# Optimization experiments

Measured on AMD Instinct MI355X. Metric: run time of the kernel, lower is better.

Reference implementation:

```python
import jax, jax.numpy as jnp
import numpy as np

B, L, C = 4, 4096, 512
G = 4            # n_groups
H = 16           # n_heads
K = 5            # offset conv kernel == offset_range_factor
GC = C // G      # n_group_channels = 128
HC = C // H      # n_head_channels = 32


def conv1d(x, w, b, pad):
    # x: [N, Cin, L], w: [Cout, Cin, K]
    out = jax.lax.conv_general_dilated(
        x, w, window_strides=(1,), padding=[(pad, pad)],
        dimension_numbers=('NCH', 'OIH', 'NCH'))
    return out + b[None, :, None]


def grid_sample_1d(feats, gy):
    # feats: [Bg, d, L]  gy: [Bg, N] normalized coords in [-1, 1]
    # bilinear, zeros padding, align_corners=False (matches F.grid_sample)
    Bg, d, Lf = feats.shape
    N = gy.shape[-1]
    iy = ((gy + 1.0) * Lf - 1.0) * 0.5
    i0 = jnp.floor(iy)
    w1 = iy - i0
    i0 = i0.astype(jnp.int32)

    def gather(idx):
        valid = ((idx >= 0) & (idx < Lf)).astype(feats.dtype)
        idxc = jnp.clip(idx, 0, Lf - 1)
        g = jnp.take_along_axis(
            feats, jnp.broadcast_to(idxc[:, None, :], (Bg, d, N)), axis=2)
        return g * valid[:, None, :]

    return gather(i0) * (1.0 - w1)[:, None, :] + gather(i0 + 1) * w1[:, None, :]


def setup_inputs() -> dict:
    key = jax.random.key(0)
    ks = jax.random.split(key, 16)
    s = 0.02
    return {
        'x':     jax.random.normal(ks[0], (B, L, C), jnp.float32),
        'Wq':    jax.random.normal(ks[1], (C, C), jnp.float32) * s,
        'bq':    jnp.zeros((C,), jnp.float32),
        'Wk':    jax.random.normal(ks[2], (C, C), jnp.float32) * s,
        'bk':    jnp.zeros((C,), jnp.float32),
        'Wv':    jax.random.normal(ks[3], (C, C), jnp.float32) * s,
        'bv':    jnp.zeros((C,), jnp.float32),
        'Woff1': jax.random.normal(ks[4], (GC, GC, K), jnp.float32) * s,
        'boff1': jnp.zeros((GC,), jnp.float32),
        'Woff2': jax.random.normal(ks[5], (1, GC, 1), jnp.float32) * s,
        'boff2': jnp.zeros((1,), jnp.float32),
        'rpb':   jax.random.normal(ks[6], (1, C, L), jnp.float32) * s,
        'Wout':  jax.random.normal(ks[7], (C, C), jnp.float32) * s,
        'bout':  jnp.zeros((C,), jnp.float32),
    }


def reference(x, Wq, bq, Wk, bk, Wv, bv, Woff1, boff1, Woff2, boff2, rpb, Wout, bout):
    Bx, Lx, Cx = x.shape
    xc = x.transpose(0, 2, 1)                                # [B, C, L]
    # 1x1 conv projections == channel matmuls
    q = jnp.einsum('oc,bcl->bol', Wq, xc) + bq[None, :, None]
    # group queries: 'b (g d) n -> (b g) d n'
    qg = q.reshape(Bx * G, GC, Lx)
    # offset prediction: conv(k=5,pad=2) then conv(k=1,pad=2) -> length L+4
    off = conv1d(qg, Woff1, boff1, pad=K // 2)               # [Bg, GC, L]
    off = conv1d(off, Woff2, boff2, pad=K // 2)[:, 0, :]     # [Bg, L+4]
    off = jnp.tanh(off) * float(K)                           # offset_range_factor
    N = off.shape[-1]
    vgrid = jnp.arange(N, dtype=x.dtype) + off               # [Bg, L+4]
    gy = 2.0 * vgrid / float(max(N - 1, 1)) - 1.0
    # bilinear gather of grouped x, then crop to L
    xg = xc.reshape(Bx * G, GC, Lx)
    xs = grid_sample_1d(xg, gy)[:, :, :Lx]                   # [Bg, GC, L]
    xs = xs.reshape(Bx, Cx, Lx)                              # '(b g) d n -> b (g d) n'
    k = jnp.einsum('oc,bcl->bol', Wk, xs) + bk[None, :, None]
    v = jnp.einsum('oc,bcl->bol', Wv, xs) + bv[None, :, None] + rpb
    # heads: [B*H, HC, L]; attention over the CHANNEL dim (i,j = head channels)
    qh = q.reshape(Bx * H, HC, Lx)
    kh = k.reshape(Bx * H, HC, Lx)
    vh = v.reshape(Bx * H, HC, Lx)
    logits = jnp.einsum('bil,bjl->bij', qh, kh) * (Cx ** -0.5)  # [BH, HC, HC]
    attn = jax.nn.softmax(logits, axis=-1)
    o = jnp.einsum('bij,bjl->bil', attn, vh)                 # [BH, HC, L]
    # '(b g) l c -> b c (g l)' with g=H, l=HC, c=L  ->  [B, L, C]
    o = o.reshape(Bx, H, HC, Lx).transpose(0, 3, 1, 2).reshape(Bx, Lx, Cx)
    return o @ Wout.T + bout
```

## Files before the change

### kernel.cpp

```cpp
#include <hip/hip_runtime.h>
#include <math.h>

#define BB   4
#define LL   4096
#define CC   512
#define GG   4
#define HH   16
#define KW   5
#define GCC  128
#define HCC  32
#define BGN  (BB*GG)
#define BHN  (BB*HH)
#define KSPLIT 16

typedef __attribute__((ext_vector_type(8))) __bf16 bf16x8;
typedef __attribute__((ext_vector_type(4))) float f32x4;

__device__ __forceinline__ unsigned int f2bf_bits(float f) {
    unsigned int u = __float_as_uint(f);
    return (u + 0x7FFFu + ((u >> 16) & 1u)) >> 16;
}
__device__ __forceinline__ float bfbits2f(unsigned int s) {
    return __uint_as_float(s << 16);
}
__device__ __forceinline__ void split2(float v, unsigned short& h, unsigned short& l) {
    unsigned int hb = f2bf_bits(v);
    float hf = bfbits2f(hb);
    unsigned int lb = f2bf_bits(v - hf);
    h = (unsigned short)hb; l = (unsigned short)lb;
}

__device__ __forceinline__ void gload16(const void* g, void* l) {
    __builtin_amdgcn_global_load_lds(
        (const __attribute__((address_space(1))) void*)g,
        (__attribute__((address_space(3))) void*)l, 16, 0, 0);
}

__global__ __launch_bounds__(256) void split_x_kernel(
    const float* __restrict__ in, unsigned short* __restrict__ hi,
    unsigned short* __restrict__ lo, int n4)
{
    int i = blockIdx.x * 256 + threadIdx.x;
    if (i >= n4) return;
    float4 v = ((const float4*)in)[i];
    ushort4 h, l;
    split2(v.x, h.x, l.x); split2(v.y, h.y, l.y);
    split2(v.z, h.z, l.z); split2(v.w, h.w, l.w);
    ((ushort4*)hi)[i] = h;
    ((ushort4*)lo)[i] = l;
}

__global__ __launch_bounds__(256) void split_w_kernel(
    const float* __restrict__ W0, const float* __restrict__ W1,
    const float* __restrict__ W2, const float* __restrict__ W3,
    unsigned short* __restrict__ hi, unsigned short* __restrict__ lo)
{
    int w = blockIdx.y;
    const float* W = (w == 0) ? W0 : (w == 1) ? W1 : (w == 2) ? W2 : W3;
    size_t seg4 = (size_t)w * 65536;
    int i = blockIdx.x * 256 + threadIdx.x;
    float4 v = ((const float4*)W)[i];
    ushort4 h, l;
    split2(v.x, h.x, l.x); split2(v.y, h.y, l.y);
    split2(v.z, h.z, l.z); split2(v.w, h.w, l.w);
    ((ushort4*)hi)[seg4 + i] = h;
    ((ushort4*)lo)[seg4 + i] = l;
}

__global__ __launch_bounds__(256) void gemm_split_mfma(
    const unsigned short* __restrict__ Ahi, const unsigned short* __restrict__ Alo,
    const unsigned short* __restrict__ Ahi2, const unsigned short* __restrict__ Alo2,
    const unsigned short* __restrict__ Bhi, const unsigned short* __restrict__ Blo,
    const float* __restrict__ bias, const float* __restrict__ bias2,
    const float* __restrict__ rpb,
    float* __restrict__ out, float* __restrict__ out2, int ySplit,
    int RA, int RB, int Kd, size_t aStride, size_t bStride, int biasOnCol)
{
    __shared__ unsigned short sm[4][4096];

    const int b  = blockIdx.z;
    const int c0 = blockIdx.x * 128;

    int rblk = blockIdx.y;
    const unsigned short* Ah_ = Ahi;
    const unsigned short* Al_ = Alo;
    const float* bias_ = bias;
    const float* rpb_  = nullptr;
    float* out_ = out;
    if (rblk >= ySplit) {
        rblk -= ySplit;
        Ah_ = Ahi2; Al_ = Alo2; bias_ = bias2; out_ = out2; rpb_ = rpb;
    }
    const int r0 = rblk * 128;

    const int tid  = threadIdx.x;
    const int lane = tid & 63;
    const int wv   = tid >> 6;
    const int wr   = wv >> 1, wc = wv & 1;

    const int srow   = lane >> 2;
    const int schunk = (lane & 3) ^ ((lane >> 3) & 3);
    const size_t laneA = (size_t)(r0 + wv * 32 + srow) * Kd + (size_t)(schunk * 8);
    const size_t laneB = (size_t)(c0 + wv * 32 + srow) * Kd + (size_t)(schunk * 8);
    const unsigned short* gAh = Ah_ + (size_t)b * aStride + laneA;
    const unsigned short* gAl = Al_ + (size_t)b * aStride + laneA;
    const unsigned short* gBh = Bhi + (size_t)b * bStride + laneB;
    const unsigned short* gBl = Blo + (size_t)b * bStride + laneB;
    const size_t rowskip = (size_t)16 * Kd;
    const int ldsOff = wv * 1024;

    const int lr = lane & 15;
    const int kx = ((lane >> 4) ^ ((lane >> 1) & 3)) * 8;
    const int aOff = (wr * 64 + lr) * 32 + kx;
    const int bOff = (wc * 64 + lr) * 32 + kx;

    f32x4 acc[4][4];
#pragma unroll
    for (int i = 0; i < 4; ++i)
#pragma unroll
        for (int j = 0; j < 4; ++j) acc[i][j] = (f32x4){0.f, 0.f, 0.f, 0.f};

    bf16x8 ah[4], al[4], bh[4], bl[4];

    for (int k0 = 0; k0 < Kd; k0 += 32) {
        gload16(gAh + k0, &sm[0][ldsOff]);
        gload16(gAh + k0 + rowskip, &sm[0][ldsOff + 512]);
        gload16(gAl + k0, &sm[1][ldsOff]);
        gload16(gAl + k0 + rowskip, &sm[1][ldsOff + 512]);
        gload16(gBh + k0, &sm[2][ldsOff]);
        gload16(gBh + k0 + rowskip, &sm[2][ldsOff + 512]);
        gload16(gBl + k0, &sm[3][ldsOff]);
        gload16(gBl + k0 + rowskip, &sm[3][ldsOff + 512]);
        __syncthreads();

        const unsigned short* mAh = &sm[0][aOff];
        const unsigned short* mAl = &sm[1][aOff];
        const unsigned short* mBh = &sm[2][bOff];
        const unsigned short* mBl = &sm[3][bOff];
#pragma unroll
        for (int i = 0; i < 4; ++i) {
            ah[i] = *(const bf16x8*)(mAh + i * 512);
            al[i] = *(const bf16x8*)(mAl + i * 512);
        }
#pragma unroll
        for (int j = 0; j < 4; ++j) {
            bh[j] = *(const bf16x8*)(mBh + j * 512);
            bl[j] = *(const bf16x8*)(mBl + j * 512);
        }
#pragma unroll
        for (int i = 0; i < 4; ++i)
#pragma unroll
            for (int j = 0; j < 4; ++j) {
                acc[i][j] = __builtin_amdgcn_mfma_f32_16x16x32_bf16(ah[i], bh[j], acc[i][j], 0, 0, 0);
                acc[i][j] = __builtin_amdgcn_mfma_f32_16x16x32_bf16(al[i], bh[j], acc[i][j], 0, 0, 0);
                acc[i][j] = __builtin_amdgcn_mfma_f32_16x16x32_bf16(ah[i], bl[j], acc[i][j], 0, 0, 0);
            }
        __syncthreads();
    }

    const int lg4 = (lane >> 4) * 4;
    float bcol[4];
#pragma unroll
    for (int fj = 0; fj < 4; ++fj)
        bcol[fj] = biasOnCol ? bias_[c0 + wc * 64 + fj * 16 + lr] : 0.f;

#pragma unroll
    for (int fi = 0; fi < 4; ++fi) {
#pragma unroll
        for (int reg = 0; reg < 4; ++reg) {
            const int r = r0 + wr * 64 + fi * 16 + lg4 + reg;
            const float br = biasOnCol ? 0.f : bias_[r];
            float* orow = out_ + ((size_t)b * RA + r) * RB + c0;
            const float* prow = rpb_ ? (rpb_ + (size_t)r * RB + c0) : nullptr;
#pragma unroll
            for (int fj = 0; fj < 4; ++fj) {
                const int c = wc * 64 + fj * 16 + lr;
                float val = acc[fi][fj][reg] + br + bcol[fj];
                if (prow) val += prow[c];
                orow[c] = val;
            }
        }
    }
}

__global__ void comb_weights(const float* __restrict__ Woff1, const float* __restrict__ boff1,
                             const float* __restrict__ Woff2, const float* __restrict__ boff2,
                             float* __restrict__ wc)
{
    int idx = blockIdx.x * 256 + threadIdx.x;
    if (idx < GCC * KW) {
        int cp = idx / KW, t = idx - cp * KW;
        float s = 0.f;
        for (int c = 0; c < GCC; ++c)
            s = fmaf(Woff2[c], Woff1[((size_t)c * GCC + cp) * KW + t], s);
        wc[idx] = s;
    } else if (idx == GCC * KW) {
        float s = boff2[0];
        for (int c = 0; c < GCC; ++c) s = fmaf(Woff2[c], boff1[c], s);
        wc[idx] = s;
    } else if (idx == GCC * KW + 1) {
        wc[idx] = boff2[0];
    }
}

#define OLT 128
__global__ __launch_bounds__(128) void offsets_part_kernel(
    const float* __restrict__ q, const float* __restrict__ wc,
    float* __restrict__ part)
{
    __shared__ float sq[32][140];
    __shared__ float sw[32 * KW];

    const int l0 = blockIdx.x * OLT;
    const int bg = blockIdx.y;
    const int cg = blockIdx.z;
    const int tid = threadIdx.x;

    const float* qb = q + ((size_t)bg * GCC + cg * 32) * LL;

    for (int i = tid; i < 32 * KW; i += 128) sw[i] = wc[cg * 32 * KW + i];

    {
        const int row = tid >> 2;
        const int l4  = tid & 3;
        const float* qrow = qb + (size_t)row * LL + l0 - 8;
        for (int j = l4; j < 34; j += 4) {
            int idx = j * 4;
            float4 v;
            if (l0 - 8 + idx >= 0) v = *(const float4*)(qrow + idx);
            else v = make_float4(0.f, 0.f, 0.f, 0.f);
            *(float4*)&sq[row][idx] = v;
        }
    }
    __syncthreads();

    const int li = tid;
    float acc = 0.f;
#pragma unroll
    for (int cp = 0; cp < 32; ++cp) {
        const float* r  = &sq[cp][li + 4];
        const float* wr = &sw[cp * KW];
        acc = fmaf(wr[0], r[0], acc);
        acc = fmaf(wr[1], r[1], acc);
        acc = fmaf(wr[2], r[2], acc);
        acc = fmaf(wr[3], r[3], acc);
        acc = fmaf(wr[4], r[4], acc);
    }
    part[((size_t)cg * BGN + bg) * LL + l0 + li] = acc;
}

__global__ __launch_bounds__(256) void offsets_finish_kernel(
    const float* __restrict__ part, const float* __restrict__ wc,
    float* __restrict__ offv)
{
    int i = blockIdx.x * 256 + threadIdx.x;
    int bg = i >> 12;
    int l  = i & (LL - 1);
    float acc;
    if (l < 2) {
        acc = wc[GCC * KW + 1];
    } else {
        acc = wc[GCC * KW]
            + part[((size_t)0 * BGN + bg) * LL + l]
            + part[((size_t)1 * BGN + bg) * LL + l]
            + part[((size_t)2 * BGN + bg) * LL + l]
            + part[((size_t)3 * BGN + bg) * LL + l];
    }
    float off = tanhf(acc) * (float)KW;
    float vg  = (float)l + off;
    float iy  = vg * ((float)LL / (float)(LL + 2 * (KW / 2) - 1)) - 0.5f;
    offv[(size_t)bg * LL + l] = iy;
}

__global__ __launch_bounds__(256) void gather_kernel(
    const float* __restrict__ x, const float* __restrict__ offv,
    unsigned short* __restrict__ xshi, unsigned short* __restrict__ xslo)
{
    int bg = blockIdx.y;
    int b = bg >> 2, g = bg & 3;
    int l  = blockIdx.x * 8 + (threadIdx.x >> 5);
    int d4 = (threadIdx.x & 31) * 4;

    float iy = offv[(size_t)bg * LL + l];
    float fi = floorf(iy);
    float w1 = iy - fi;
    int i0 = (int)fi;
    int i1 = i0 + 1;

    const float* xb = x + (size_t)b * LL * CC + (size_t)g * GCC + d4;
    float4 v0 = make_float4(0.f, 0.f, 0.f, 0.f);
    float4 v1 = make_float4(0.f, 0.f, 0.f, 0.f);
    if (i0 >= 0 && i0 < LL) v0 = *(const float4*)(xb + (size_t)i0 * CC);
    if (i1 >= 0 && i1 < LL) v1 = *(const float4*)(xb + (size_t)i1 * CC);
    float w0 = 1.f - w1;
    float4 r = make_float4(v0.x * w0 + v1.x * w1, v0.y * w0 + v1.y * w1,
                           v0.z * w0 + v1.z * w1, v0.w * w0 + v1.w * w1);
    size_t o = ((size_t)b * LL + l) * CC + (size_t)g * GCC + d4;
    ushort4 h, lo4;
    split2(r.x, h.x, lo4.x); split2(r.y, h.y, lo4.y);
    split2(r.z, h.z, lo4.z); split2(r.w, h.w, lo4.w);
    *(ushort4*)(xshi + o) = h;
    *(ushort4*)(xslo + o) = lo4;
}

__global__ __launch_bounds__(64) void qk_logits(
    const float* __restrict__ q, const float* __restrict__ k,
    float* __restrict__ part)
{
    int ks = blockIdx.x, bh = blockIdx.y;
    int b = bh >> 4, h = bh & 15;
    int lane = threadIdx.x;
    int ti = lane >> 3, tj = lane & 7;
    const float* qb = q + ((size_t)b * CC + h * HCC + ti * 4) * LL;
    const float* kb = k + ((size_t)b * CC + h * HCC + tj * 4) * LL;

    float acc[4][4];
#pragma unroll
    for (int i = 0; i < 4; ++i)
#pragma unroll
        for (int j = 0; j < 4; ++j) acc[i][j] = 0.f;

    const int chunk = LL / KSPLIT;
    int l0 = ks * chunk;
    for (int l = l0; l < l0 + chunk; l += 8) {
        float4 qa[4][2], kv[4][2];
#pragma unroll
        for (int p = 0; p < 4; ++p) {
            qa[p][0] = *(const float4*)(qb + (size_t)p * LL + l);
            qa[p][1] = *(const float4*)(qb + (size_t)p * LL + l + 4);
            kv[p][0] = *(const float4*)(kb + (size_t)p * LL + l);
            kv[p][1] = *(const float4*)(kb + (size_t)p * LL + l + 4);
        }
#pragma unroll
        for (int i = 0; i < 4; ++i)
#pragma unroll
            for (int j = 0; j < 4; ++j) {
                float s = acc[i][j];
                s = fmaf(qa[i][0].x, kv[j][0].x, s);
                s = fmaf(qa[i][0].y, kv[j][0].y, s);
                s = fmaf(qa[i][0].z, kv[j][0].z, s);
                s = fmaf(qa[i][0].w, kv[j][0].w, s);
                s = fmaf(qa[i][1].x, kv[j][1].x, s);
                s = fmaf(qa[i][1].y, kv[j][1].y, s);
                s = fmaf(qa[i][1].z, kv[j][1].z, s);
                s = fmaf(qa[i][1].w, kv[j][1].w, s);
                acc[i][j] = s;
            }
    }
#pragma unroll
    for (int i = 0; i < 4; ++i)
#pragma unroll
        for (int j = 0; j < 4; ++j)
            part[(((size_t)bh * KSPLIT + ks) * HCC + ti * 4 + i) * HCC + tj * 4 + j] = acc[i][j];
}

__global__ __launch_bounds__(64) void softmax_kernel(
    const float* __restrict__ part, float* __restrict__ attn)
{
    int bh = blockIdx.x;
    int i = threadIdx.x;
    if (i >= HCC) return;
    const float SCALE = 0.044194173824159216f;

    float lg[HCC];
    float mx = -1e30f;
#pragma unroll
    for (int j = 0; j < HCC; ++j) {
        float s = 0.f;
        for (int ks = 0; ks < KSPLIT; ++ks)
            s += part[(((size_t)bh * KSPLIT + ks) * HCC + i) * HCC + j];
        s *= SCALE;
        lg[j] = s;
        mx = fmaxf(mx, s);
    }
    float sum = 0.f;
#pragma unroll
    for (int j = 0; j < HCC; ++j) {
        float e = expf(lg[j] - mx);
        lg[j] = e;
        sum += e;
    }
    float inv = 1.f / sum;
#pragma unroll
    for (int j = 0; j < HCC; ++j)
        attn[((size_t)bh * HCC + i) * HCC + j] = lg[j] * inv;
}

__global__ __launch_bounds__(256) void attn_v_kernel(
    const float* __restrict__ attn, const float* __restrict__ v,
    unsigned short* __restrict__ ohi, unsigned short* __restrict__ olo)
{
    int bh = blockIdx.y;
    int b = bh >> 4, h = bh & 15;
    int tid = threadIdx.x;
    int i = tid >> 3, lsub = tid & 7;

    float arow[HCC];
#pragma unroll
    for (int j = 0; j < HCC; ++j)
        arow[j] = attn[((size_t)bh * HCC + i) * HCC + j];

    const float* vb = v + ((size_t)b * CC + h * HCC) * LL;
    __shared__ float os[HCC][65];

    for (int l0 = blockIdx.x * 512; l0 < blockIdx.x * 512 + 512; l0 += 64) {
        int lbase = l0 + lsub * 8;
        float4 a0 = make_float4(0.f, 0.f, 0.f, 0.f);
        float4 a1 = make_float4(0.f, 0.f, 0.f, 0.f);
#pragma unroll 8
        for (int j = 0; j < HCC; ++j) {
            float aw = arow[j];
            float4 v0 = *(const float4*)(vb + (size_t)j * LL + lbase);
            float4 v1 = *(const float4*)(vb + (size_t)j * LL + lbase + 4);
            a0.x = fmaf(aw, v0.x, a0.x); a0.y = fmaf(aw, v0.y, a0.y);
            a0.z = fmaf(aw, v0.z, a0.z); a0.w = fmaf(aw, v0.w, a0.w);
            a1.x = fmaf(aw, v1.x, a1.x); a1.y = fmaf(aw, v1.y, a1.y);
            a1.z = fmaf(aw, v1.z, a1.z); a1.w = fmaf(aw, v1.w, a1.w);
        }
        os[i][lsub*8+0] = a0.x; os[i][lsub*8+1] = a0.y;
        os[i][lsub*8+2] = a0.z; os[i][lsub*8+3] = a0.w;
        os[i][lsub*8+4] = a1.x; os[i][lsub*8+5] = a1.y;
        os[i][lsub*8+6] = a1.z; os[i][lsub*8+7] = a1.w;
        __syncthreads();
        int i2 = tid & 31, lw = tid >> 5;
#pragma unroll
        for (int c = 0; c < 8; ++c) {
            int ll = lw * 8 + c;
            float val = os[i2][ll];
            unsigned short hbits, lbits;
            split2(val, hbits, lbits);
            size_t oidx = ((size_t)b * LL + l0 + ll) * CC + h * HCC + i2;
            ohi[oidx] = hbits;
            olo[oidx] = lbits;
        }
        __syncthreads();
    }
}

extern "C" void kernel_launch(void* const* d_in, const int* in_sizes, int n_in,
                              void* d_out, int out_size, void* d_ws, size_t ws_size,
                              hipStream_t stream)
{
    (void)in_sizes; (void)n_in; (void)out_size; (void)ws_size;
    const float* x     = (const float*)d_in[0];
    const float* Wq    = (const float*)d_in[1];
    const float* bq    = (const float*)d_in[2];
    const float* Wk    = (const float*)d_in[3];
    const float* bk    = (const float*)d_in[4];
    const float* Wv    = (const float*)d_in[5];
    const float* bv    = (const float*)d_in[6];
    const float* Woff1 = (const float*)d_in[7];
    const float* boff1 = (const float*)d_in[8];
    const float* Woff2 = (const float*)d_in[9];
    const float* boff2 = (const float*)d_in[10];
    const float* rpb   = (const float*)d_in[11];
    const float* Wout  = (const float*)d_in[12];
    const float* bout  = (const float*)d_in[13];
    float* out = (float*)d_out;

    float* ws = (float*)d_ws;
    float* q    = ws;
    float* kbuf = ws + 8388608;
    float* vbuf = ws + 16777216;
    unsigned short* dhi = (unsigned short*)(ws + 25165824);
    unsigned short* dlo = (unsigned short*)(ws + 25165824 + 4194304);
    unsigned short* whi = (unsigned short*)(ws + 33554432);
    unsigned short* wlo = (unsigned short*)(ws + 33554432 + 524288);
    float* offv = ws + 34603008;
    float* wcmb = ws + 34668544;
    float* part = ws + 34669568;
    float* attn = ws + 35718144;

    const size_t NK = (size_t)LL * CC;
    const int NOSPLIT = 1 << 20;

    comb_weights<<<dim3(3), dim3(256), 0, stream>>>(Woff1, boff1, Woff2, boff2, wcmb);
    split_w_kernel<<<dim3(256, 4), dim3(256), 0, stream>>>(Wq, Wk, Wv, Wout, whi, wlo);
    split_x_kernel<<<dim3(8192), dim3(256), 0, stream>>>(x, dhi, dlo, 2097152);

    gemm_split_mfma<<<dim3(32, 4, 4), dim3(256), 0, stream>>>(
        whi + 0 * 262144, wlo + 0 * 262144, whi, wlo, dhi, dlo,
        bq, bq, nullptr, q, q, NOSPLIT,
        CC, LL, CC, 0, NK, 0);

    offsets_part_kernel<<<dim3(32, 16, 4), dim3(128), 0, stream>>>(q, wcmb, part);
    offsets_finish_kernel<<<dim3(256), dim3(256), 0, stream>>>(part, wcmb, offv);
    gather_kernel<<<dim3(512, 16), dim3(256), 0, stream>>>(x, offv, dhi, dlo);

    gemm_split_mfma<<<dim3(32, 8, 4), dim3(256), 0, stream>>>(
        whi + 1 * 262144, wlo + 1 * 262144,
        whi + 2 * 262144, wlo + 2 * 262144,
        dhi, dlo, bk, bv, rpb, kbuf, vbuf, 4,
        CC, LL, CC, 0, NK, 0);

    qk_logits<<<dim3(KSPLIT, BHN), dim3(64), 0, stream>>>(q, kbuf, part);
    softmax_kernel<<<dim3(BHN), dim3(64), 0, stream>>>(part, attn);
    attn_v_kernel<<<dim3(8, BHN), dim3(256), 0, stream>>>(attn, vbuf, dhi, dlo);

    gemm_split_mfma<<<dim3(4, 32, 4), dim3(256), 0, stream>>>(
        dhi, dlo, dhi, dlo, whi + 3 * 262144, wlo + 3 * 262144,
        bout, bout, nullptr, out, out, NOSPLIT,
        LL, CC, CC, NK, 0, 1);
}
```

Before: 401.4 us.

## Double-buffer LDS in split-bf16 GEMM to overlap global loads with MFMA

Doubles the shared-memory tile buffer and prefetches two K-steps ahead. Manual vmcnt waits and barriers let the global-to-LDS loads for step t+2 run while the MFMA work for step t executes. This is meant to hide global memory latency in the GEMM main loop. In exchange, LDS use per block doubles, which may lower occupancy, and the hand-written waitcnt counts must match the exact number of outstanding loads.

```diff
diff --git a/kernel.cpp b/kernel.cpp
--- a/kernel.cpp
+++ b/kernel.cpp
@@ -76,7 +76,7 @@
     float* __restrict__ out, float* __restrict__ out2, int ySplit,
     int RA, int RB, int Kd, size_t aStride, size_t bStride, int biasOnCol)
 {
-    __shared__ unsigned short sm[4][4096];
+    __shared__ unsigned short sm[2 * 4 * 4096];
 
     const int b  = blockIdx.z;
     const int c0 = blockIdx.x * 128;
@@ -122,41 +122,70 @@
 
     bf16x8 ah[4], al[4], bh[4], bl[4];
 
-    for (int k0 = 0; k0 < Kd; k0 += 32) {
-        gload16(gAh + k0, &sm[0][ldsOff]);
-        gload16(gAh + k0 + rowskip, &sm[0][ldsOff + 512]);
-        gload16(gAl + k0, &sm[1][ldsOff]);
-        gload16(gAl + k0 + rowskip, &sm[1][ldsOff + 512]);
-        gload16(gBh + k0, &sm[2][ldsOff]);
-        gload16(gBh + k0 + rowskip, &sm[2][ldsOff + 512]);
-        gload16(gBl + k0, &sm[3][ldsOff]);
-        gload16(gBl + k0 + rowskip, &sm[3][ldsOff + 512]);
-        __syncthreads();
-
-        const unsigned short* mAh = &sm[0][aOff];
-        const unsigned short* mAl = &sm[1][aOff];
-        const unsigned short* mBh = &sm[2][bOff];
-        const unsigned short* mBl = &sm[3][bOff];
-#pragma unroll
-        for (int i = 0; i < 4; ++i) {
-            ah[i] = *(const bf16x8*)(mAh + i * 512);
-            al[i] = *(const bf16x8*)(mAl + i * 512);
-        }
-#pragma unroll
-        for (int j = 0; j < 4; ++j) {
-            bh[j] = *(const bf16x8*)(mBh + j * 512);
-            bl[j] = *(const bf16x8*)(mBl + j * 512);
-        }
-#pragma unroll
-        for (int i = 0; i < 4; ++i)
-#pragma unroll
-            for (int j = 0; j < 4; ++j) {
-                acc[i][j] = __builtin_amdgcn_mfma_f32_16x16x32_bf16(ah[i], bh[j], acc[i][j], 0, 0, 0);
-                acc[i][j] = __builtin_amdgcn_mfma_f32_16x16x32_bf16(al[i], bh[j], acc[i][j], 0, 0, 0);
-                acc[i][j] = __builtin_amdgcn_mfma_f32_16x16x32_bf16(ah[i], bl[j], acc[i][j], 0, 0, 0);
-            }
-        __syncthreads();
-    }
+#define STAGE(bufbase, k0)                                                    \
+    {                                                                         \
+        unsigned short* d0 = &sm[(bufbase) + 0 * 4096 + ldsOff];              \
+        gload16(gAh + (k0), d0);  gload16(gAh + (k0) + rowskip, d0 + 512);    \
+        unsigned short* d1 = &sm[(bufbase) + 1 * 4096 + ldsOff];              \
+        gload16(gAl + (k0), d1);  gload16(gAl + (k0) + rowskip, d1 + 512);    \
+        unsigned short* d2 = &sm[(bufbase) + 2 * 4096 + ldsOff];              \
+        gload16(gBh + (k0), d2);  gload16(gBh + (k0) + rowskip, d2 + 512);    \
+        unsigned short* d3 = &sm[(bufbase) + 3 * 4096 + ldsOff];              \
+        gload16(gBl + (k0), d3);  gload16(gBl + (k0) + rowskip, d3 + 512);    \
+    }
+
+#define LOADF(bufbase)                                                        \
+    {                                                                         \
+        const unsigned short* mAh = &sm[(bufbase) + 0 * 4096 + aOff];         \
+        const unsigned short* mAl = &sm[(bufbase) + 1 * 4096 + aOff];         \
+        const unsigned short* mBh = &sm[(bufbase) + 2 * 4096 + bOff];         \
+        const unsigned short* mBl = &sm[(bufbase) + 3 * 4096 + bOff];         \
+        _Pragma("unroll")                                                     \
+        for (int i = 0; i < 4; ++i) {                                         \
+            ah[i] = *(const bf16x8*)(mAh + i * 512);                          \
+            al[i] = *(const bf16x8*)(mAl + i * 512);                          \
+        }                                                                     \
+        _Pragma("unroll")                                                     \
+        for (int j = 0; j < 4; ++j) {                                         \
+            bh[j] = *(const bf16x8*)(mBh + j * 512);                          \
+            bl[j] = *(const bf16x8*)(mBl + j * 512);                          \
+        }                                                                     \
+    }
+
+#define DOMFMA                                                                \
+    {                                                                         \
+        _Pragma("unroll")                                                     \
+        for (int i = 0; i < 4; ++i)                                           \
+            _Pragma("unroll")                                                 \
+            for (int j = 0; j < 4; ++j) {                                     \
+                acc[i][j] = __builtin_amdgcn_mfma_f32_16x16x32_bf16(ah[i], bh[j], acc[i][j], 0, 0, 0); \
+                acc[i][j] = __builtin_amdgcn_mfma_f32_16x16x32_bf16(al[i], bh[j], acc[i][j], 0, 0, 0); \
+                acc[i][j] = __builtin_amdgcn_mfma_f32_16x16x32_bf16(ah[i], bl[j], acc[i][j], 0, 0, 0); \
+            }                                                                 \
+    }
+
+    const int nt = Kd >> 5;
+    STAGE(0, 0)
+    STAGE(16384, 32)
+
+    int cur = 0;
+    for (int t = 0; t < nt; ++t) {
+        const int bufb = cur ? 16384 : 0;
+        if (t < nt - 1) asm volatile("s_waitcnt vmcnt(8)" ::: "memory");
+        else            asm volatile("s_waitcnt vmcnt(0)" ::: "memory");
+        __builtin_amdgcn_s_barrier();
+        LOADF(bufb)
+        asm volatile("s_waitcnt lgkmcnt(0)" ::: "memory");
+        __builtin_amdgcn_sched_barrier(0);
+        __builtin_amdgcn_s_barrier();
+        if (t + 2 < nt) STAGE(bufb, (t + 2) * 32)
+        DOMFMA
+        cur ^= 1;
+    }
+
+#undef STAGE
+#undef LOADF
+#undef DOMFMA
 
     const int lg4 = (lane >> 4) * 4;
     float bcol[4];
```

Measured after the change: 396.0 us. Within noise of the previous version (-1.3%).
